# Kernel tuning notes

Hardware: AMD Instinct MI355X
Metric: run time of the kernel (lower is better)

## Reference

```python
import jax, jax.numpy as jnp
import numpy as np

TAU = 1.0
NUM_CLASSES = 14
LOSS_WEIGHT = 1.0
KERNEL_SUM = 26.0  # 3x3x3 ones with center zeroed


def setup_inputs() -> dict:
    key = jax.random.key(0)
    k1, k2, k3 = jax.random.split(key, 3)
    B, C, H, W, D = 2, NUM_CLASSES, 96, 96, 96
    preds_S = jax.random.normal(k1, (B, C, H, W, D), dtype=jnp.float32)
    preds_T = jax.random.normal(k2, (B, C, H, W, D), dtype=jnp.float32)
    gt_labels = jax.random.randint(k3, (B, 1, H, W, D), 0, NUM_CLASSES, dtype=jnp.int64)
    return {"preds_S": preds_S, "preds_T": preds_T, "gt_labels": gt_labels}


def _boundary_masks(gt_labels):
    # gt_labels: [B,1,H,W,D] int -> boundary mask per (batch, class): [B, nc, H*W*D]
    B = gt_labels.shape[0]
    H, W, D = gt_labels.shape[2:]
    kernel = jnp.ones((1, 1, 3, 3, 3), jnp.float32).at[0, 0, 1, 1, 1].set(0.0)
    onehot = (gt_labels[:, 0, None, :, :, :] ==
              jnp.arange(NUM_CLASSES)[None, :, None, None, None]).astype(jnp.float32)  # [B,nc,H,W,D]
    x = onehot.reshape(B * NUM_CLASSES, 1, H, W, D)
    conv = jax.lax.conv_general_dilated(x, kernel, (1, 1, 1), 'SAME')  # NCHWD
    conv = conv.reshape(B, NUM_CLASSES, H * W * D)
    # boundary[conv==26]=0 ; boundary[conv>0]=1
    return jnp.where(conv == KERNEL_SUM, 0.0, jnp.where(conv > 0.0, 1.0, 0.0))


def reference(preds_S, preds_T, gt_labels):
    B, C = preds_S.shape[0], preds_S.shape[1]
    boundary = _boundary_masks(gt_labels)                      # [B, nc, P]
    S = preds_S.reshape(B, C, -1) / TAU                        # [B, C, P]
    T = preds_T.reshape(B, C, -1) / TAU
    logS = jax.nn.log_softmax(S, axis=1)
    pT = jax.nn.softmax(T, axis=1)
    # per-voxel KL summed over classes (softmax is over class dim, same for every cls loop)
    kl_pos = jnp.sum(pT * (jnp.log(pT) - logS), axis=1)        # [B, P]
    count = boundary.sum(axis=-1)                              # [B, nc] boundary voxels
    num = jnp.einsum('bkp,bp->bk', boundary, kl_pos)           # [B, nc]
    # F.kl_div default reduction='mean' divides by C * n_boundary elements
    loss_bk = jnp.where(count > 0.0, num / (C * count), 0.0)
    return LOSS_WEIGHT * loss_bk.sum()
```

## Files before the change

kernel.cpp:

```cpp
#include <hip/hip_runtime.h>

#define NC 14
#define DIM 96
#define PP (DIM*DIM*DIM)
#define QPB (PP/4)
#define NBLOCKS (2*QPB/256)

__global__ __launch_bounds__(256) void bkd_main(
    const float* __restrict__ S, const float* __restrict__ T,
    const int* __restrict__ lab,
    double* __restrict__ gnum, int* __restrict__ gcnt)
{
    const int tid = threadIdx.x;
    const unsigned q  = blockIdx.x * 256u + tid;
    const unsigned b  = q / QPB;
    const unsigned qi = q - b * QPB;
    const int p = (int)(qi * 4u);
    const int d = p % DIM;
    const int t = p / DIM;
    const int w = t % DIM;
    const int h = t / DIM;

    const float* Tb = T + (size_t)b * NC * PP + p;
    const float* Sb = S + (size_t)b * NC * PP + p;
    float ZT0=0,ZT1=0,ZT2=0,ZT3=0, ZS0=0,ZS1=0,ZS2=0,ZS3=0, A0=0,A1=0,A2=0,A3=0;
#pragma unroll
    for (int c = 0; c < NC; ++c) {
        const float4 t4 = *(const float4*)(Tb + (size_t)c * PP);
        const float4 s4 = *(const float4*)(Sb + (size_t)c * PP);
        const float u0 = __expf(t4.x), u1 = __expf(t4.y), u2 = __expf(t4.z), u3 = __expf(t4.w);
        ZT0 += u0; ZT1 += u1; ZT2 += u2; ZT3 += u3;
        ZS0 += __expf(s4.x); ZS1 += __expf(s4.y); ZS2 += __expf(s4.z); ZS3 += __expf(s4.w);
        A0 = fmaf(u0, t4.x - s4.x, A0);
        A1 = fmaf(u1, t4.y - s4.y, A1);
        A2 = fmaf(u2, t4.z - s4.z, A2);
        A3 = fmaf(u3, t4.w - s4.w, A3);
    }
    const float kl0 = A0 / ZT0 + __logf(ZS0) - __logf(ZT0);
    const float kl1 = A1 / ZT1 + __logf(ZS1) - __logf(ZT1);
    const float kl2 = A2 / ZT2 + __logf(ZS2) - __logf(ZT2);
    const float kl3 = A3 / ZT3 + __logf(ZS3) - __logf(ZT3);

    const int lbase = (int)b * PP;
    unsigned m0 = 0, m1 = 0, m2 = 0, m3 = 0;
#pragma unroll
    for (int dh = -1; dh <= 1; ++dh) {
        const int hh = h + dh;
        if ((unsigned)hh >= (unsigned)DIM) continue;
#pragma unroll
        for (int dw = -1; dw <= 1; ++dw) {
            const int ww = w + dw;
            if ((unsigned)ww >= (unsigned)DIM) continue;
            const int* rp = lab + lbase + (hh * DIM + ww) * DIM + d;
            const int4 v = *(const int4*)rp;
            const unsigned a0 = 1u << v.x, a1 = 1u << v.y, a2 = 1u << v.z, a3 = 1u << v.w;
            const unsigned mla = (d > 0)        ? (1u << rp[-1]) : 0u;
            const unsigned mlb = (d < DIM - 4)  ? (1u << rp[4])  : 0u;
            if (dh == 0 && dw == 0) {
                m0 |= mla | a1;  m1 |= a0 | a2;  m2 |= a1 | a3;  m3 |= a2 | mlb;
            } else {
                const unsigned s01 = a0 | a1, s12 = a1 | a2, s23 = a2 | a3;
                m0 |= mla | s01;  m1 |= s01 | a2;  m2 |= s12 | a3;  m3 |= s23 | mlb;
            }
        }
    }

    const bool hwi = (h >= 1 && h <= DIM - 2 && w >= 1 && w <= DIM - 2);
    const unsigned mc0 = (hwi && d > 0       && (m0 & (m0 - 1)) == 0) ? 0u : m0;
    const unsigned mc1 = (hwi                && (m1 & (m1 - 1)) == 0) ? 0u : m1;
    const unsigned mc2 = (hwi                && (m2 & (m2 - 1)) == 0) ? 0u : m2;
    const unsigned mc3 = (hwi && d < DIM - 4 && (m3 & (m3 - 1)) == 0) ? 0u : m3;

    float lnum[NC];
    int   lcnt[NC];
#pragma unroll
    for (int k = 0; k < NC; ++k) {
        const unsigned bit = 1u << k;
        const int c0 = (mc0 & bit) ? 1 : 0, c1 = (mc1 & bit) ? 1 : 0,
                  c2 = (mc2 & bit) ? 1 : 0, c3 = (mc3 & bit) ? 1 : 0;
        lcnt[k] = c0 + c1 + c2 + c3;
        lnum[k] = ((mc0 & bit) ? kl0 : 0.f) + ((mc1 & bit) ? kl1 : 0.f)
                + ((mc2 & bit) ? kl2 : 0.f) + ((mc3 & bit) ? kl3 : 0.f);
    }

#pragma unroll
    for (int k = 0; k < NC; ++k) {
        float v = lnum[k];
        int   c = lcnt[k];
#pragma unroll
        for (int off = 32; off > 0; off >>= 1) {
            v += __shfl_down(v, off, 64);
            c += __shfl_down(c, off, 64);
        }
        lnum[k] = v; lcnt[k] = c;
    }

    __shared__ float s_num[NC];
    __shared__ int   s_cnt[NC];
    if (tid < NC) { s_num[tid] = 0.f; s_cnt[tid] = 0; }
    __syncthreads();
    if ((tid & 63) == 0) {
#pragma unroll
        for (int k = 0; k < NC; ++k) {
            atomicAdd(&s_num[k], lnum[k]);
            atomicAdd(&s_cnt[k], lcnt[k]);
        }
    }
    __syncthreads();
    if (tid < NC) {
        atomicAdd(&gnum[b * NC + tid], (double)s_num[tid]);
        atomicAdd(&gcnt[b * NC + tid], s_cnt[tid]);
    }
}

__global__ void bkd_final(const double* __restrict__ gnum,
                          const int* __restrict__ gcnt,
                          float* __restrict__ out)
{
    const int i = threadIdx.x;
    double term = 0.0;
    if (i < 2 * NC) {
        const int c = gcnt[i];
        if (c > 0) term = gnum[i] / ((double)NC * (double)c);
    }
#pragma unroll
    for (int off = 32; off > 0; off >>= 1)
        term += __shfl_down(term, off, 64);
    if (i == 0) out[0] = (float)term;
}

extern "C" void kernel_launch(void* const* d_in, const int* in_sizes, int n_in,
                              void* d_out, int out_size, void* d_ws, size_t ws_size,
                              hipStream_t stream) {
    const float* S  = (const float*)d_in[0];
    const float* T  = (const float*)d_in[1];
    const int* lab  = (const int*)d_in[2];
    float* out      = (float*)d_out;

    double* gnum = (double*)d_ws;
    int*    gcnt = (int*)((char*)d_ws + 2 * NC * sizeof(double));

    hipMemsetAsync(d_ws, 0, 2 * NC * (sizeof(double) + sizeof(int)), stream);

    bkd_main<<<NBLOCKS, 256, 0, stream>>>(S, T, lab, gnum, gcnt);
    bkd_final<<<1, 64, 0, stream>>>(gnum, gcnt, out);
}
```

Measured before the change: 251.2 us.

## Split each voxel quad across four lanes with shuffle-combined class and stencil work

Each group of four threads now shares one 4-voxel quad. Each lane loads a subset of the 14 class channels, and partial softmax sums are combined with xor shuffles. The 3x3 label stencil rows are likewise split across the lanes and OR-reduced. Each lane then owns one voxel, so the per-class reduction becomes a ballot/popcount for counts plus a single float butterfly, instead of 14 float+int reductions. This raises memory-level parallelism with four times more threads and fewer loads per thread, at the cost of extra shuffles and a 4x larger grid.

```diff
diff --git a/kernel.cpp b/kernel.cpp
--- a/kernel.cpp
+++ b/kernel.cpp
@@ -3,8 +3,7 @@
 #define NC 14
 #define DIM 96
 #define PP (DIM*DIM*DIM)
-#define QPB (PP/4)
-#define NBLOCKS (2*QPB/256)
+#define BLOCKS_PER_B 3456
 
 __global__ __launch_bounds__(256) void bkd_main(
     const float* __restrict__ S, const float* __restrict__ T,
@@ -12,9 +11,10 @@
     double* __restrict__ gnum, int* __restrict__ gcnt)
 {
     const int tid = threadIdx.x;
-    const unsigned q  = blockIdx.x * 256u + tid;
-    const unsigned b  = q / QPB;
-    const unsigned qi = q - b * QPB;
+    const int j   = tid & 3;
+    const unsigned bq = blockIdx.x;
+    const unsigned b  = bq / BLOCKS_PER_B;
+    const unsigned qi = (bq - b * BLOCKS_PER_B) * 64u + (unsigned)(tid >> 2);
     const int p = (int)(qi * 4u);
     const int d = p % DIM;
     const int t = p / DIM;
@@ -23,87 +23,94 @@
 
     const float* Tb = T + (size_t)b * NC * PP + p;
     const float* Sb = S + (size_t)b * NC * PP + p;
+    const int cD = 12 + (j & 1);
+    const float w4 = (j < 2) ? 1.f : 0.f;
+    const float4 tA = *(const float4*)(Tb + (size_t)(j)      * PP);
+    const float4 sA = *(const float4*)(Sb + (size_t)(j)      * PP);
+    const float4 tB = *(const float4*)(Tb + (size_t)(4 + j)  * PP);
+    const float4 sB = *(const float4*)(Sb + (size_t)(4 + j)  * PP);
+    const float4 tC = *(const float4*)(Tb + (size_t)(8 + j)  * PP);
+    const float4 sC = *(const float4*)(Sb + (size_t)(8 + j)  * PP);
+    const float4 tD = *(const float4*)(Tb + (size_t)cD       * PP);
+    const float4 sD = *(const float4*)(Sb + (size_t)cD       * PP);
+
     float ZT0=0,ZT1=0,ZT2=0,ZT3=0, ZS0=0,ZS1=0,ZS2=0,ZS3=0, A0=0,A1=0,A2=0,A3=0;
-#pragma unroll
-    for (int c = 0; c < NC; ++c) {
-        const float4 t4 = *(const float4*)(Tb + (size_t)c * PP);
-        const float4 s4 = *(const float4*)(Sb + (size_t)c * PP);
-        const float u0 = __expf(t4.x), u1 = __expf(t4.y), u2 = __expf(t4.z), u3 = __expf(t4.w);
-        ZT0 += u0; ZT1 += u1; ZT2 += u2; ZT3 += u3;
-        ZS0 += __expf(s4.x); ZS1 += __expf(s4.y); ZS2 += __expf(s4.z); ZS3 += __expf(s4.w);
-        A0 = fmaf(u0, t4.x - s4.x, A0);
-        A1 = fmaf(u1, t4.y - s4.y, A1);
-        A2 = fmaf(u2, t4.z - s4.z, A2);
-        A3 = fmaf(u3, t4.w - s4.w, A3);
+#define ACC(t4, s4, wgt)                                                     \
+    {                                                                        \
+        const float u0 = __expf(t4.x) * (wgt), u1 = __expf(t4.y) * (wgt),    \
+                    u2 = __expf(t4.z) * (wgt), u3 = __expf(t4.w) * (wgt);    \
+        ZT0 += u0; ZT1 += u1; ZT2 += u2; ZT3 += u3;                          \
+        ZS0 += __expf(s4.x) * (wgt); ZS1 += __expf(s4.y) * (wgt);            \
+        ZS2 += __expf(s4.z) * (wgt); ZS3 += __expf(s4.w) * (wgt);            \
+        A0 = fmaf(u0, t4.x - s4.x, A0); A1 = fmaf(u1, t4.y - s4.y, A1);      \
+        A2 = fmaf(u2, t4.z - s4.z, A2); A3 = fmaf(u3, t4.w - s4.w, A3);      \
     }
-    const float kl0 = A0 / ZT0 + __logf(ZS0) - __logf(ZT0);
-    const float kl1 = A1 / ZT1 + __logf(ZS1) - __logf(ZT1);
-    const float kl2 = A2 / ZT2 + __logf(ZS2) - __logf(ZT2);
-    const float kl3 = A3 / ZT3 + __logf(ZS3) - __logf(ZT3);
+    ACC(tA, sA, 1.f) ACC(tB, sB, 1.f) ACC(tC, sC, 1.f) ACC(tD, sD, w4)
+#undef ACC
+
+#define BFLY(v) v += __shfl_xor(v, 1, 64); v += __shfl_xor(v, 2, 64);
+    BFLY(ZT0) BFLY(ZT1) BFLY(ZT2) BFLY(ZT3)
+    BFLY(ZS0) BFLY(ZS1) BFLY(ZS2) BFLY(ZS3)
+    BFLY(A0)  BFLY(A1)  BFLY(A2)  BFLY(A3)
+#undef BFLY
+
+    const float Aj  = (j == 0) ? A0  : (j == 1) ? A1  : (j == 2) ? A2  : A3;
+    const float ZTj = (j == 0) ? ZT0 : (j == 1) ? ZT1 : (j == 2) ? ZT2 : ZT3;
+    const float ZSj = (j == 0) ? ZS0 : (j == 1) ? ZS1 : (j == 2) ? ZS2 : ZS3;
+    const float kl  = Aj / ZTj + __logf(ZSj) - __logf(ZTj);
 
     const int lbase = (int)b * PP;
     unsigned m0 = 0, m1 = 0, m2 = 0, m3 = 0;
-#pragma unroll
-    for (int dh = -1; dh <= 1; ++dh) {
-        const int hh = h + dh;
-        if ((unsigned)hh >= (unsigned)DIM) continue;
-#pragma unroll
-        for (int dw = -1; dw <= 1; ++dw) {
-            const int ww = w + dw;
-            if ((unsigned)ww >= (unsigned)DIM) continue;
-            const int* rp = lab + lbase + (hh * DIM + ww) * DIM + d;
-            const int4 v = *(const int4*)rp;
-            const unsigned a0 = 1u << v.x, a1 = 1u << v.y, a2 = 1u << v.z, a3 = 1u << v.w;
-            const unsigned mla = (d > 0)        ? (1u << rp[-1]) : 0u;
-            const unsigned mlb = (d < DIM - 4)  ? (1u << rp[4])  : 0u;
-            if (dh == 0 && dw == 0) {
-                m0 |= mla | a1;  m1 |= a0 | a2;  m2 |= a1 | a3;  m3 |= a2 | mlb;
-            } else {
-                const unsigned s01 = a0 | a1, s12 = a1 | a2, s23 = a2 | a3;
-                m0 |= mla | s01;  m1 |= s01 | a2;  m2 |= s12 | a3;  m3 |= s23 | mlb;
-            }
-        }
+#define DOROW(rw)                                                            \
+    {                                                                        \
+        const int dh = (rw) / 3 - 1, dw = (rw) % 3 - 1;                      \
+        const int hh = h + dh, ww = w + dw;                                  \
+        if ((unsigned)hh < (unsigned)DIM && (unsigned)ww < (unsigned)DIM) {  \
+            const int* rp = lab + lbase + (hh * DIM + ww) * DIM + d;         \
+            const int4 v = *(const int4*)rp;                                 \
+            const unsigned a0 = 1u << v.x, a1 = 1u << v.y,                   \
+                           a2 = 1u << v.z, a3 = 1u << v.w;                   \
+            const unsigned mla = (d > 0)       ? (1u << rp[-1]) : 0u;        \
+            const unsigned mlb = (d < DIM - 4) ? (1u << rp[4])  : 0u;        \
+            if ((rw) == 4) {                                                 \
+                m0 |= mla | a1; m1 |= a0 | a2; m2 |= a1 | a3; m3 |= a2 | mlb;\
+            } else {                                                         \
+                const unsigned s01 = a0|a1, s12 = a1|a2, s23 = a2|a3;        \
+                m0 |= mla|s01; m1 |= s01|a2; m2 |= s12|a3; m3 |= s23|mlb;    \
+            }                                                                \
+        }                                                                    \
     }
+    DOROW(j)
+    DOROW(j + 4)
+    if (j == 3) DOROW(8)
+#undef DOROW
+
+#define BOR(m) m |= __shfl_xor(m, 1, 64); m |= __shfl_xor(m, 2, 64);
+    BOR(m0) BOR(m1) BOR(m2) BOR(m3)
+#undef BOR
 
     const bool hwi = (h >= 1 && h <= DIM - 2 && w >= 1 && w <= DIM - 2);
-    const unsigned mc0 = (hwi && d > 0       && (m0 & (m0 - 1)) == 0) ? 0u : m0;
-    const unsigned mc1 = (hwi                && (m1 & (m1 - 1)) == 0) ? 0u : m1;
-    const unsigned mc2 = (hwi                && (m2 & (m2 - 1)) == 0) ? 0u : m2;
-    const unsigned mc3 = (hwi && d < DIM - 4 && (m3 & (m3 - 1)) == 0) ? 0u : m3;
-
-    float lnum[NC];
-    int   lcnt[NC];
-#pragma unroll
-    for (int k = 0; k < NC; ++k) {
-        const unsigned bit = 1u << k;
-        const int c0 = (mc0 & bit) ? 1 : 0, c1 = (mc1 & bit) ? 1 : 0,
-                  c2 = (mc2 & bit) ? 1 : 0, c3 = (mc3 & bit) ? 1 : 0;
-        lcnt[k] = c0 + c1 + c2 + c3;
-        lnum[k] = ((mc0 & bit) ? kl0 : 0.f) + ((mc1 & bit) ? kl1 : 0.f)
-                + ((mc2 & bit) ? kl2 : 0.f) + ((mc3 & bit) ? kl3 : 0.f);
-    }
-
-#pragma unroll
-    for (int k = 0; k < NC; ++k) {
-        float v = lnum[k];
-        int   c = lcnt[k];
-#pragma unroll
-        for (int off = 32; off > 0; off >>= 1) {
-            v += __shfl_down(v, off, 64);
-            c += __shfl_down(c, off, 64);
-        }
-        lnum[k] = v; lcnt[k] = c;
-    }
+    const bool din = (j == 0) ? (d > 0) : (j == 3) ? (d < DIM - 4) : true;
+    unsigned mj = (j == 0) ? m0 : (j == 1) ? m1 : (j == 2) ? m2 : m3;
+    if (hwi && din && (mj & (mj - 1)) == 0) mj = 0;
 
     __shared__ float s_num[NC];
     __shared__ int   s_cnt[NC];
     if (tid < NC) { s_num[tid] = 0.f; s_cnt[tid] = 0; }
     __syncthreads();
-    if ((tid & 63) == 0) {
+
+    const int lane0 = ((tid & 63) == 0);
 #pragma unroll
-        for (int k = 0; k < NC; ++k) {
-            atomicAdd(&s_num[k], lnum[k]);
-            atomicAdd(&s_cnt[k], lcnt[k]);
+    for (int k = 0; k < NC; ++k) {
+        const unsigned bit = 1u << k;
+        const unsigned long long bal = __ballot(mj & bit);
+        float v = (mj & bit) ? kl : 0.f;
+#pragma unroll
+        for (int off = 32; off > 0; off >>= 1)
+            v += __shfl_xor(v, off, 64);
+        if (lane0) {
+            atomicAdd(&s_num[k], v);
+            atomicAdd(&s_cnt[k], (int)__popcll(bal));
         }
     }
     __syncthreads();
@@ -142,6 +149,6 @@
 
     hipMemsetAsync(d_ws, 0, 2 * NC * (sizeof(double) + sizeof(int)), stream);
 
-    bkd_main<<<NBLOCKS, 256, 0, stream>>>(S, T, lab, gnum, gcnt);
+    bkd_main<<<2 * BLOCKS_PER_B, 256, 0, stream>>>(S, T, lab, gnum, gcnt);
     bkd_final<<<1, 64, 0, stream>>>(gnum, gcnt, out);
 }
```

After: 289.4 us. +15.2%, slower.

## Process eight voxels per thread and rotate class order per block

Applied to the files above, without the earlier changes.

Each thread now handles eight consecutive voxels instead of four, so the per-thread wave reductions, shared and global atomics, and label-neighbour loads are amortised over twice as many voxels, with half as many blocks. The class loop start is rotated per block so that concurrent blocks hit different class planes, which is meant to spread DRAM channel traffic. A launch-bounds occupancy hint of four blocks is added. The cost is higher register pressure and fewer threads in flight for hiding memory latency on this bandwidth-bound kernel.

```diff
diff --git a/kernel.cpp b/kernel.cpp
--- a/kernel.cpp
+++ b/kernel.cpp
@@ -3,19 +3,19 @@
 #define NC 14
 #define DIM 96
 #define PP (DIM*DIM*DIM)
-#define QPB (PP/4)
-#define NBLOCKS (2*QPB/256)
+#define VPT 8
+#define VPB (256*VPT)
+#define BLOCKS_PER_B (PP/VPB)
 
-__global__ __launch_bounds__(256) void bkd_main(
+__global__ __launch_bounds__(256, 4) void bkd_main(
     const float* __restrict__ S, const float* __restrict__ T,
     const int* __restrict__ lab,
     double* __restrict__ gnum, int* __restrict__ gcnt)
 {
     const int tid = threadIdx.x;
-    const unsigned q  = blockIdx.x * 256u + tid;
-    const unsigned b  = q / QPB;
-    const unsigned qi = q - b * QPB;
-    const int p = (int)(qi * 4u);
+    const unsigned bq = blockIdx.x;
+    const unsigned b  = bq / BLOCKS_PER_B;
+    const int p = (int)((bq - b * BLOCKS_PER_B) * VPB) + tid * VPT;
     const int d = p % DIM;
     const int t = p / DIM;
     const int w = t % DIM;
@@ -23,26 +23,41 @@
 
     const float* Tb = T + (size_t)b * NC * PP + p;
     const float* Sb = S + (size_t)b * NC * PP + p;
-    float ZT0=0,ZT1=0,ZT2=0,ZT3=0, ZS0=0,ZS1=0,ZS2=0,ZS3=0, A0=0,A1=0,A2=0,A3=0;
+
+    float ZT[VPT], ZS[VPT], A[VPT];
 #pragma unroll
-    for (int c = 0; c < NC; ++c) {
-        const float4 t4 = *(const float4*)(Tb + (size_t)c * PP);
-        const float4 s4 = *(const float4*)(Sb + (size_t)c * PP);
-        const float u0 = __expf(t4.x), u1 = __expf(t4.y), u2 = __expf(t4.z), u3 = __expf(t4.w);
-        ZT0 += u0; ZT1 += u1; ZT2 += u2; ZT3 += u3;
-        ZS0 += __expf(s4.x); ZS1 += __expf(s4.y); ZS2 += __expf(s4.z); ZS3 += __expf(s4.w);
-        A0 = fmaf(u0, t4.x - s4.x, A0);
-        A1 = fmaf(u1, t4.y - s4.y, A1);
-        A2 = fmaf(u2, t4.z - s4.z, A2);
-        A3 = fmaf(u3, t4.w - s4.w, A3);
+    for (int i = 0; i < VPT; ++i) { ZT[i] = 0.f; ZS[i] = 0.f; A[i] = 0.f; }
+
+    const int rot = (int)(bq % NC);
+#pragma unroll
+    for (int cc = 0; cc < NC; ++cc) {
+        int c = cc + rot; if (c >= NC) c -= NC;
+        const size_t off = (size_t)c * PP;
+        const float4 t0 = *(const float4*)(Tb + off);
+        const float4 t1 = *(const float4*)(Tb + off + 4);
+        const float4 s0 = *(const float4*)(Sb + off);
+        const float4 s1 = *(const float4*)(Sb + off + 4);
+        const float tv[VPT] = {t0.x, t0.y, t0.z, t0.w, t1.x, t1.y, t1.z, t1.w};
+        const float sv[VPT] = {s0.x, s0.y, s0.z, s0.w, s1.x, s1.y, s1.z, s1.w};
+#pragma unroll
+        for (int i = 0; i < VPT; ++i) {
+            const float u = __expf(tv[i]);
+            ZT[i] += u;
+            ZS[i] += __expf(sv[i]);
+            A[i]   = fmaf(u, tv[i] - sv[i], A[i]);
+        }
     }
-    const float kl0 = A0 / ZT0 + __logf(ZS0) - __logf(ZT0);
-    const float kl1 = A1 / ZT1 + __logf(ZS1) - __logf(ZT1);
-    const float kl2 = A2 / ZT2 + __logf(ZS2) - __logf(ZT2);
-    const float kl3 = A3 / ZT3 + __logf(ZS3) - __logf(ZT3);
+
+    float kl[VPT];
+#pragma unroll
+    for (int i = 0; i < VPT; ++i)
+        kl[i] = A[i] / ZT[i] + __logf(ZS[i]) - __logf(ZT[i]);
 
     const int lbase = (int)b * PP;
-    unsigned m0 = 0, m1 = 0, m2 = 0, m3 = 0;
+    unsigned mk[VPT];
+#pragma unroll
+    for (int i = 0; i < VPT; ++i) mk[i] = 0u;
+
 #pragma unroll
     for (int dh = -1; dh <= 1; ++dh) {
         const int hh = h + dh;
@@ -52,35 +67,46 @@
             const int ww = w + dw;
             if ((unsigned)ww >= (unsigned)DIM) continue;
             const int* rp = lab + lbase + (hh * DIM + ww) * DIM + d;
-            const int4 v = *(const int4*)rp;
-            const unsigned a0 = 1u << v.x, a1 = 1u << v.y, a2 = 1u << v.z, a3 = 1u << v.w;
-            const unsigned mla = (d > 0)        ? (1u << rp[-1]) : 0u;
-            const unsigned mlb = (d < DIM - 4)  ? (1u << rp[4])  : 0u;
+            const int4 v0 = *(const int4*)rp;
+            const int4 v1 = *(const int4*)(rp + 4);
+            unsigned lb[VPT + 2];
+            lb[0] = (d > 0)       ? (1u << rp[-1]) : 0u;
+            lb[1] = 1u << v0.x;  lb[2] = 1u << v0.y;
+            lb[3] = 1u << v0.z;  lb[4] = 1u << v0.w;
+            lb[5] = 1u << v1.x;  lb[6] = 1u << v1.y;
+            lb[7] = 1u << v1.z;  lb[8] = 1u << v1.w;
+            lb[9] = (d < DIM - VPT) ? (1u << rp[VPT]) : 0u;
             if (dh == 0 && dw == 0) {
-                m0 |= mla | a1;  m1 |= a0 | a2;  m2 |= a1 | a3;  m3 |= a2 | mlb;
+#pragma unroll
+                for (int i = 0; i < VPT; ++i) mk[i] |= lb[i] | lb[i + 2];
             } else {
-                const unsigned s01 = a0 | a1, s12 = a1 | a2, s23 = a2 | a3;
-                m0 |= mla | s01;  m1 |= s01 | a2;  m2 |= s12 | a3;  m3 |= s23 | mlb;
+#pragma unroll
+                for (int i = 0; i < VPT; ++i) mk[i] |= lb[i] | lb[i + 1] | lb[i + 2];
             }
         }
     }
 
     const bool hwi = (h >= 1 && h <= DIM - 2 && w >= 1 && w <= DIM - 2);
-    const unsigned mc0 = (hwi && d > 0       && (m0 & (m0 - 1)) == 0) ? 0u : m0;
-    const unsigned mc1 = (hwi                && (m1 & (m1 - 1)) == 0) ? 0u : m1;
-    const unsigned mc2 = (hwi                && (m2 & (m2 - 1)) == 0) ? 0u : m2;
-    const unsigned mc3 = (hwi && d < DIM - 4 && (m3 & (m3 - 1)) == 0) ? 0u : m3;
+#pragma unroll
+    for (int i = 0; i < VPT; ++i) {
+        const int dd = d + i;
+        const bool din = (dd > 0) && (dd < DIM - 1);
+        if (hwi && din && (mk[i] & (mk[i] - 1)) == 0u) mk[i] = 0u;
+    }
 
     float lnum[NC];
     int   lcnt[NC];
 #pragma unroll
-    for (int k = 0; k < NC; ++k) {
-        const unsigned bit = 1u << k;
-        const int c0 = (mc0 & bit) ? 1 : 0, c1 = (mc1 & bit) ? 1 : 0,
-                  c2 = (mc2 & bit) ? 1 : 0, c3 = (mc3 & bit) ? 1 : 0;
-        lcnt[k] = c0 + c1 + c2 + c3;
-        lnum[k] = ((mc0 & bit) ? kl0 : 0.f) + ((mc1 & bit) ? kl1 : 0.f)
-                + ((mc2 & bit) ? kl2 : 0.f) + ((mc3 & bit) ? kl3 : 0.f);
+    for (int k = 0; k < NC; ++k) { lnum[k] = 0.f; lcnt[k] = 0; }
+#pragma unroll
+    for (int i = 0; i < VPT; ++i) {
+        const float kv = kl[i];
+        const unsigned mm = mk[i];
+#pragma unroll
+        for (int k = 0; k < NC; ++k) {
+            lnum[k] += (mm & (1u << k)) ? kv : 0.f;
+            lcnt[k] += (mm >> k) & 1u;
+        }
     }
 
 #pragma unroll
@@ -142,6 +168,6 @@
 
     hipMemsetAsync(d_ws, 0, 2 * NC * (sizeof(double) + sizeof(int)), stream);
 
-    bkd_main<<<NBLOCKS, 256, 0, stream>>>(S, T, lab, gnum, gcnt);
+    bkd_main<<<2 * BLOCKS_PER_B, 256, 0, stream>>>(S, T, lab, gnum, gcnt);
     bkd_final<<<1, 64, 0, stream>>>(gnum, gcnt, out);
 }
```

After: 433.5 us. 72.6% more time.
